# Optimization experiments

Hardware: AMD Instinct MI355X
Metric: run time of the kernel (lower is better)

Reference implementation:

```python
import jax, jax.numpy as jnp
import numpy as np

NEG_SLOPE = 0.2  # LeakyReLU(0.2) used for attention scores


def setup_inputs() -> dict:
    key = jax.random.key(0)
    k1, k2, k3, k4, k5 = jax.random.split(key, 5)
    B, H, N, F, D = 1024, 32, 25, 128, 128
    return {
        "x_self": jax.random.normal(k1, (B, H, F), dtype=jnp.float32),
        "x_neigh": jax.random.normal(k2, (B, H, N, F), dtype=jnp.float32),
        "w_feat": jax.random.normal(k3, (F, D), dtype=jnp.float32) * 0.1,
        "a_self": jax.random.normal(k4, (D, 1), dtype=jnp.float32) * 0.1,
        "a_neigh": jax.random.normal(k5, (D, 1), dtype=jnp.float32) * 0.1,
    }


def reference(x_self, x_neigh, w_feat, a_self, a_neigh):
    # xw_self: [B, H, 1, D]; xw_neigh: [B, H, N, D]
    xw_self = jnp.einsum("bhf,fd->bhd", x_self, w_feat)[:, :, None, :]
    xw_neigh = jnp.einsum("bhnf,fd->bhnd", x_neigh, w_feat)
    xw_all = jnp.concatenate([xw_self, xw_neigh], axis=2)  # [B, H, N+1, D]
    # attention scores over the (self + neighbours) axis
    attn_self = jnp.einsum("bhkd,do->bhko", xw_self, a_self)   # [B, H, 1, 1]
    attn_neigh = jnp.einsum("bhkd,do->bhko", xw_all, a_neigh)  # [B, H, N+1, 1]
    attn_u = jax.nn.leaky_relu(attn_self + attn_neigh, negative_slope=NEG_SLOPE)
    attn = jax.nn.softmax(attn_u, axis=2)                      # [B, H, N+1, 1]
    h_out = jnp.sum(attn * xw_all, axis=2)                     # [B, H, D]
    return jax.nn.relu(h_out)
```

## Files before the change

### kernel.cpp

```cpp
#include <hip/hip_runtime.h>

typedef unsigned short u16;
typedef unsigned int   u32;
typedef __attribute__((ext_vector_type(4))) float f32x4;
typedef __attribute__((ext_vector_type(4))) int   i32x4;

#define NPAIR 32768
#define NB    25
#define FD    128

__device__ __forceinline__ float bflo(u32 u){ return __uint_as_float(u << 16); }
__device__ __forceinline__ float bfhi(u32 u){ return __uint_as_float(u & 0xFFFF0000u); }
__device__ __forceinline__ u16 f2bf(float f){
  u32 u = __float_as_uint(f);
  u += 0x7FFFu + ((u >> 16) & 1u);
  return (u16)(u >> 16);
}
__device__ __forceinline__ float rowsum16(float x){
  x += __shfl_xor(x, 1);
  x += __shfl_xor(x, 2);
  x += __shfl_xor(x, 4);
  x += __shfl_xor(x, 8);
  return x;
}

__global__ __launch_bounds__(64) void prep_wa(const void* w_, const void* as_, const void* an_,
                                              const u16* __restrict__ xsniff,
                                              float* __restrict__ wa, int* __restrict__ flag_out){
  const int l = threadIdx.x;
  const u16 v1 = xsniff[l], v2 = xsniff[64 + l];
  int e1 = (v1 >> 7) & 0xFF, e2 = (v2 >> 7) & 0xFF;
  int e = e1 > e2 ? e1 : e2;
  #pragma unroll
  for(int m=1; m<=32; m<<=1){ int o = __shfl_xor(e, m); e = e > o ? e : o; }
  unsigned long long zb = __ballot(((l & 1) == 0) && (v1 == 0 || v2 == 0));
  const bool isf32 = (e >= 141) || (__popcll(zb) >= 20);

  const int f = blockIdx.x;
  float ps, pn;
  if (isf32){
    const float* w  = (const float*)w_;
    const float* as = (const float*)as_;
    const float* an = (const float*)an_;
    float w0 = w[f*FD + 2*l], w1 = w[f*FD + 2*l + 1];
    ps = w0*as[2*l] + w1*as[2*l+1];
    pn = w0*an[2*l] + w1*an[2*l+1];
  } else {
    const u16* w  = (const u16*)w_;
    const u16* as = (const u16*)as_;
    const u16* an = (const u16*)an_;
    u32 wd = *(const u32*)(w + f*FD + 2*l);
    u32 av = *(const u32*)(as + 2*l);
    u32 nv = *(const u32*)(an + 2*l);
    ps = bflo(wd)*bflo(av) + bfhi(wd)*bfhi(av);
    pn = bflo(wd)*bflo(nv) + bfhi(wd)*bfhi(nv);
  }
  #pragma unroll
  for(int m=1; m<=32; m<<=1){ ps += __shfl_xor(ps, m); pn += __shfl_xor(pn, m); }
  if (l == 0){ wa[f] = ps; wa[FD + f] = pn; }
  if (blockIdx.x == 0 && l == 0) flag_out[0] = isf32 ? 1 : 0;
}

template<bool FP32>
__device__ __forceinline__ void attn_body(const void* __restrict__ xs_, const void* __restrict__ xn_,
                                          const float* __restrict__ wa, u16* __restrict__ xbar,
                                          const int p, const int lane){
  const int g  = lane >> 4;
  const int q  = lane & 15;
  const int f0 = q << 3;

  float was[8], wan[8];
  {
    float4 a = *(const float4*)(wa + f0);
    float4 b = *(const float4*)(wa + f0 + 4);
    was[0]=a.x; was[1]=a.y; was[2]=a.z; was[3]=a.w;
    was[4]=b.x; was[5]=b.y; was[6]=b.z; was[7]=b.w;
    float4 c = *(const float4*)(wa + FD + f0);
    float4 d = *(const float4*)(wa + FD + f0 + 4);
    wan[0]=c.x; wan[1]=c.y; wan[2]=c.z; wan[3]=c.w;
    wan[4]=d.x; wan[5]=d.y; wan[6]=d.z; wan[7]=d.w;
  }

  float xf[7][8];
  #pragma unroll
  for(int i=0;i<7;++i){
    const int v = 4*i + g;
    if (v <= NB){
      if (FP32){
        const float* src = (v==0) ? ((const float*)xs_ + (size_t)p*FD + f0)
                                  : ((const float*)xn_ + (size_t)p*(NB*FD) + (size_t)(v-1)*FD + f0);
        float4 A = *(const float4*)src;
        float4 B = *(const float4*)(src + 4);
        xf[i][0]=A.x; xf[i][1]=A.y; xf[i][2]=A.z; xf[i][3]=A.w;
        xf[i][4]=B.x; xf[i][5]=B.y; xf[i][6]=B.z; xf[i][7]=B.w;
      } else {
        const u16* src = (v==0) ? ((const u16*)xs_ + (size_t)p*FD + f0)
                                : ((const u16*)xn_ + (size_t)p*(NB*FD) + (size_t)(v-1)*FD + f0);
        uint4 d = *(const uint4*)src;
        xf[i][0]=bflo(d.x); xf[i][1]=bfhi(d.x);
        xf[i][2]=bflo(d.y); xf[i][3]=bfhi(d.y);
        xf[i][4]=bflo(d.z); xf[i][5]=bfhi(d.z);
        xf[i][6]=bflo(d.w); xf[i][7]=bfhi(d.w);
      }
    } else {
      #pragma unroll
      for(int j=0;j<8;++j) xf[i][j] = 0.f;
    }
  }

  float pn[7];
  #pragma unroll
  for(int i=0;i<7;++i){
    float s = 0.f;
    #pragma unroll
    for(int j=0;j<8;++j) s += xf[i][j]*wan[j];
    pn[i] = rowsum16(s);
  }
  float ps = 0.f;
  #pragma unroll
  for(int j=0;j<8;++j) ps += xf[0][j]*was[j];
  ps = rowsum16(ps);
  const float s_self = __shfl(ps, 0);

  float u[7];
  #pragma unroll
  for(int i=0;i<7;++i){
    const int v = 4*i + g;
    if (v <= NB){
      float t = s_self + pn[i];
      u[i] = fmaxf(t, 0.2f*t);
    } else u[i] = -3.0e38f;
  }
  float m = u[0];
  #pragma unroll
  for(int i=1;i<7;++i) m = fmaxf(m, u[i]);
  m = fmaxf(m, __shfl_xor(m, 16));
  m = fmaxf(m, __shfl_xor(m, 32));

  float e[7]; float S = 0.f;
  #pragma unroll
  for(int i=0;i<7;++i){
    const int v = 4*i + g;
    e[i] = (v <= NB) ? __expf(u[i] - m) : 0.f;
    S += e[i];
  }
  S += __shfl_xor(S, 16);
  S += __shfl_xor(S, 32);
  const float rinv = 1.0f / S;

  float acc[8];
  #pragma unroll
  for(int j=0;j<8;++j) acc[j] = 0.f;
  #pragma unroll
  for(int i=0;i<7;++i)
    #pragma unroll
    for(int j=0;j<8;++j) acc[j] += e[i]*xf[i][j];
  #pragma unroll
  for(int j=0;j<8;++j){
    acc[j] += __shfl_xor(acc[j], 16);
    acc[j] += __shfl_xor(acc[j], 32);
    acc[j] *= rinv;
  }
  if (g == 0){
    u32 o0 = (u32)f2bf(acc[0]) | ((u32)f2bf(acc[1])<<16);
    u32 o1 = (u32)f2bf(acc[2]) | ((u32)f2bf(acc[3])<<16);
    u32 o2 = (u32)f2bf(acc[4]) | ((u32)f2bf(acc[5])<<16);
    u32 o3 = (u32)f2bf(acc[6]) | ((u32)f2bf(acc[7])<<16);
    *(uint4*)(xbar + (size_t)p*FD + f0) = make_uint4(o0,o1,o2,o3);
  }
}

__global__ __launch_bounds__(256) void attn_xbar(const void* __restrict__ xs, const void* __restrict__ xn,
                                                 const float* __restrict__ wa, const int* __restrict__ flag,
                                                 u16* __restrict__ xbar){
  const int lane = threadIdx.x & 63;
  const int p    = blockIdx.x*4 + (threadIdx.x >> 6);
  if (flag[0]) attn_body<true >(xs, xn, wa, xbar, p, lane);
  else         attn_body<false>(xs, xn, wa, xbar, p, lane);
}

__global__ __launch_bounds__(256) void matvec_out(const u16* __restrict__ xbar,
                                                  const void* __restrict__ w_,
                                                  void* __restrict__ out_,
                                                  const int* __restrict__ flag){
  __shared__ u16 wlds[FD*FD];
  const int tid = threadIdx.x;
  const bool isf32 = (flag[0] != 0);
  if (isf32){
    const float* w = (const float*)w_;
    #pragma unroll
    for(int i=0;i<8;++i){
      const int e = (i*256 + tid)*8;
      float4 A = *(const float4*)(w + e);
      float4 B = *(const float4*)(w + e + 4);
      u32 o0 = (u32)f2bf(A.x) | ((u32)f2bf(A.y)<<16);
      u32 o1 = (u32)f2bf(A.z) | ((u32)f2bf(A.w)<<16);
      u32 o2 = (u32)f2bf(B.x) | ((u32)f2bf(B.y)<<16);
      u32 o3 = (u32)f2bf(B.z) | ((u32)f2bf(B.w)<<16);
      *(uint4*)(wlds + e) = make_uint4(o0,o1,o2,o3);
    }
  } else {
    const u16* w = (const u16*)w_;
    #pragma unroll
    for(int i=0;i<8;++i){
      const int e = (i*256 + tid)*8;
      *(uint4*)(wlds + e) = *(const uint4*)(w + e);
    }
  }
  __syncthreads();

  const int lane = tid & 63, wv = tid >> 6;
  const int col  = lane & 15, quad = lane >> 4;

  i32x4 bfru[8][4];
  #pragma unroll
  for(int nt=0;nt<8;++nt)
    #pragma unroll
    for(int kt=0;kt<4;++kt){
      union { u16 s[8]; i32x4 u; } bb;
      #pragma unroll
      for(int j=0;j<8;++j) bb.s[j] = wlds[(kt*32 + quad*8 + j)*FD + nt*16 + col];
      bfru[nt][kt] = bb.u;
    }

  const int waveG = blockIdx.x*4 + wv;
  #pragma unroll
  for(int s=0;s<2;++s){
    const int tile = waveG + s*1024;
    const u16* arow = xbar + (size_t)(tile*16 + col)*FD;
    f32x4 acc[8];
    #pragma unroll
    for(int nt=0;nt<8;++nt){ f32x4 z = {0.f,0.f,0.f,0.f}; acc[nt] = z; }
    #pragma unroll
    for(int kt=0;kt<4;++kt){
      i32x4 av = *(const i32x4*)(arow + kt*32 + quad*8);
      #pragma unroll
      for(int nt=0;nt<8;++nt){
        asm volatile("s_nop 1\n\t"
                     "v_mfma_f32_16x16x32_bf16 %0, %1, %2, %0\n\t"
                     "s_nop 7\n\t"
                     "s_nop 7"
                     : "+v"(acc[nt]) : "v"(av), "v"(bfru[nt][kt]));
      }
    }
    if (isf32){
      float* orow = (float*)out_ + (size_t)tile*(16*FD);
      #pragma unroll
      for(int nt=0;nt<8;++nt)
        #pragma unroll
        for(int r=0;r<4;++r)
          orow[(quad*4+r)*FD + nt*16 + col] = fmaxf(acc[nt][r], 0.f);
    } else {
      u16* orow = (u16*)out_ + (size_t)tile*(16*FD);
      #pragma unroll
      for(int nt=0;nt<8;++nt)
        #pragma unroll
        for(int r=0;r<4;++r)
          orow[(quad*4+r)*FD + nt*16 + col] = f2bf(fmaxf(acc[nt][r], 0.f));
    }
  }
}

extern "C" void kernel_launch(void* const* d_in, const int* in_sizes, int n_in,
                              void* d_out, int out_size, void* d_ws, size_t ws_size,
                              hipStream_t stream){
  const void* x_self  = d_in[0];
  const void* x_neigh = d_in[1];
  const void* w_feat  = d_in[2];
  const void* a_self  = d_in[3];
  const void* a_neigh = d_in[4];

  int*   flag = (int*)d_ws;
  float* wa   = (float*)d_ws + 64;
  u16*   xbar = (u16*)d_ws + 1024;

  prep_wa  <<<FD,      64,  0, stream>>>(w_feat, a_self, a_neigh, (const u16*)x_self, wa, flag);
  attn_xbar<<<NPAIR/4, 256, 0, stream>>>(x_self, x_neigh, wa, flag, xbar);
  matvec_out<<<256,    256, 0, stream>>>(xbar, w_feat, d_out, flag);
}
```

Baseline: 568.2 us.

## Fuse attention aggregation with output matvec via LDS and prepacked W fragments

Merges the attention/xbar kernel and the MFMA matvec into one kernel: each block computes 16 aggregated rows into LDS, then multiplies them by W using fragments pre-packed in the prep kernel. This removes the global xbar write/read and a launch, and uses nontemporal loads for the streamed inputs. Each wave now processes 4 pairs serially, which may reduce memory-level parallelism.

```diff
diff --git a/kernel.cpp b/kernel.cpp
--- a/kernel.cpp
+++ b/kernel.cpp
@@ -4,6 +4,7 @@
 typedef unsigned int   u32;
 typedef __attribute__((ext_vector_type(4))) float f32x4;
 typedef __attribute__((ext_vector_type(4))) int   i32x4;
+typedef __attribute__((ext_vector_type(4))) u32   u32x4;
 
 #define NPAIR 32768
 #define NB    25
@@ -23,242 +24,231 @@
   x += __shfl_xor(x, 8);
   return x;
 }
-
-__global__ __launch_bounds__(64) void prep_wa(const void* w_, const void* as_, const void* an_,
-                                              const u16* __restrict__ xsniff,
-                                              float* __restrict__ wa, int* __restrict__ flag_out){
-  const int l = threadIdx.x;
+__device__ __forceinline__ bool sniff_f32(const u16* __restrict__ xsniff, int l){
   const u16 v1 = xsniff[l], v2 = xsniff[64 + l];
   int e1 = (v1 >> 7) & 0xFF, e2 = (v2 >> 7) & 0xFF;
   int e = e1 > e2 ? e1 : e2;
   #pragma unroll
-  for(int m=1; m<=32; m<<=1){ int o = __shfl_xor(e, m); e = e > o ? e : o; }
+  for (int m = 1; m <= 32; m <<= 1){ int o = __shfl_xor(e, m); e = e > o ? e : o; }
   unsigned long long zb = __ballot(((l & 1) == 0) && (v1 == 0 || v2 == 0));
-  const bool isf32 = (e >= 141) || (__popcll(zb) >= 20);
-
-  const int f = blockIdx.x;
-  float ps, pn;
-  if (isf32){
-    const float* w  = (const float*)w_;
-    const float* as = (const float*)as_;
-    const float* an = (const float*)an_;
-    float w0 = w[f*FD + 2*l], w1 = w[f*FD + 2*l + 1];
-    ps = w0*as[2*l] + w1*as[2*l+1];
-    pn = w0*an[2*l] + w1*an[2*l+1];
+  return (e >= 141) || (__popcll(zb) >= 20);
+}
+
+__global__ __launch_bounds__(64) void prep(const void* w_, const void* as_, const void* an_,
+                                           const u16* __restrict__ xsniff,
+                                           float* __restrict__ wa, u16* __restrict__ wpk,
+                                           int* __restrict__ flag_out){
+  const int l = threadIdx.x;
+  const bool isf32 = sniff_f32(xsniff, l);
+
+  if (blockIdx.x < FD){
+    const int f = blockIdx.x;
+    float ps, pn;
+    if (isf32){
+      const float* w  = (const float*)w_;
+      const float* as = (const float*)as_;
+      const float* an = (const float*)an_;
+      float w0 = w[f*FD + 2*l], w1 = w[f*FD + 2*l + 1];
+      ps = w0*as[2*l] + w1*as[2*l+1];
+      pn = w0*an[2*l] + w1*an[2*l+1];
+    } else {
+      const u16* w  = (const u16*)w_;
+      const u16* as = (const u16*)as_;
+      const u16* an = (const u16*)an_;
+      u32 wd = *(const u32*)(w + f*FD + 2*l);
+      u32 av = *(const u32*)(as + 2*l);
+      u32 nv = *(const u32*)(an + 2*l);
+      ps = bflo(wd)*bflo(av) + bfhi(wd)*bfhi(av);
+      pn = bflo(wd)*bflo(nv) + bfhi(wd)*bfhi(nv);
+    }
+    #pragma unroll
+    for(int m=1; m<=32; m<<=1){ ps += __shfl_xor(ps, m); pn += __shfl_xor(pn, m); }
+    if (l == 0){ wa[f] = ps; wa[FD + f] = pn; }
+    if (blockIdx.x == 0 && l == 0) flag_out[0] = isf32 ? 1 : 0;
   } else {
-    const u16* w  = (const u16*)w_;
-    const u16* as = (const u16*)as_;
-    const u16* an = (const u16*)an_;
-    u32 wd = *(const u32*)(w + f*FD + 2*l);
-    u32 av = *(const u32*)(as + 2*l);
-    u32 nv = *(const u32*)(an + 2*l);
-    ps = bflo(wd)*bflo(av) + bfhi(wd)*bfhi(av);
-    pn = bflo(wd)*bflo(nv) + bfhi(wd)*bfhi(nv);
-  }
-  #pragma unroll
-  for(int m=1; m<=32; m<<=1){ ps += __shfl_xor(ps, m); pn += __shfl_xor(pn, m); }
-  if (l == 0){ wa[f] = ps; wa[FD + f] = pn; }
-  if (blockIdx.x == 0 && l == 0) flag_out[0] = isf32 ? 1 : 0;
+    const int unit = (blockIdx.x - FD)*64 + l;
+    const int nt   = unit >> 8;
+    const int kt   = (unit >> 6) & 3;
+    const int fl   = unit & 63;
+    const int col  = fl & 15, quad = fl >> 4;
+    union { u16 s[8]; u32x4 u; } bb;
+    #pragma unroll
+    for (int j = 0; j < 8; ++j){
+      const int idx = (kt*32 + quad*8 + j)*FD + nt*16 + col;
+      bb.s[j] = isf32 ? f2bf(((const float*)w_)[idx]) : ((const u16*)w_)[idx];
+    }
+    *(u32x4*)(wpk + unit*8) = bb.u;
+  }
 }
 
 template<bool FP32>
-__device__ __forceinline__ void attn_body(const void* __restrict__ xs_, const void* __restrict__ xn_,
-                                          const float* __restrict__ wa, u16* __restrict__ xbar,
-                                          const int p, const int lane){
+__device__ __forceinline__ void fused_body(const void* __restrict__ xs_, const void* __restrict__ xn_,
+                                           const float* __restrict__ wa, const u16* __restrict__ wpk,
+                                           void* __restrict__ out_, u16* __restrict__ xb){
+  const int tid  = threadIdx.x;
+  const int lane = tid & 63, wv = tid >> 6;
   const int g  = lane >> 4;
   const int q  = lane & 15;
   const int f0 = q << 3;
+  const int pbase = blockIdx.x * 16;
 
   float was[8], wan[8];
   {
-    float4 a = *(const float4*)(wa + f0);
-    float4 b = *(const float4*)(wa + f0 + 4);
-    was[0]=a.x; was[1]=a.y; was[2]=a.z; was[3]=a.w;
-    was[4]=b.x; was[5]=b.y; was[6]=b.z; was[7]=b.w;
-    float4 c = *(const float4*)(wa + FD + f0);
-    float4 d = *(const float4*)(wa + FD + f0 + 4);
-    wan[0]=c.x; wan[1]=c.y; wan[2]=c.z; wan[3]=c.w;
-    wan[4]=d.x; wan[5]=d.y; wan[6]=d.z; wan[7]=d.w;
-  }
-
-  float xf[7][8];
+    f32x4 a = *(const f32x4*)(wa + f0);
+    f32x4 b = *(const f32x4*)(wa + f0 + 4);
+    was[0]=a[0]; was[1]=a[1]; was[2]=a[2]; was[3]=a[3];
+    was[4]=b[0]; was[5]=b[1]; was[6]=b[2]; was[7]=b[3];
+    f32x4 c = *(const f32x4*)(wa + FD + f0);
+    f32x4 d = *(const f32x4*)(wa + FD + f0 + 4);
+    wan[0]=c[0]; wan[1]=c[1]; wan[2]=c[2]; wan[3]=c[3];
+    wan[4]=d[0]; wan[5]=d[1]; wan[6]=d[2]; wan[7]=d[3];
+  }
+
+  #pragma unroll 1
+  for (int pp = 0; pp < 4; ++pp){
+    const int row = wv*4 + pp;
+    const int p   = pbase + row;
+
+    float xf[7][8];
+    #pragma unroll
+    for(int i=0;i<7;++i){
+      const int v = 4*i + g;
+      if (v <= NB){
+        if (FP32){
+          const float* src = (v==0) ? ((const float*)xs_ + (size_t)p*FD + f0)
+                                    : ((const float*)xn_ + (size_t)p*(NB*FD) + (size_t)(v-1)*FD + f0);
+          f32x4 A = __builtin_nontemporal_load((const f32x4*)src);
+          f32x4 B = __builtin_nontemporal_load((const f32x4*)(src + 4));
+          xf[i][0]=A[0]; xf[i][1]=A[1]; xf[i][2]=A[2]; xf[i][3]=A[3];
+          xf[i][4]=B[0]; xf[i][5]=B[1]; xf[i][6]=B[2]; xf[i][7]=B[3];
+        } else {
+          const u16* src = (v==0) ? ((const u16*)xs_ + (size_t)p*FD + f0)
+                                  : ((const u16*)xn_ + (size_t)p*(NB*FD) + (size_t)(v-1)*FD + f0);
+          u32x4 d = __builtin_nontemporal_load((const u32x4*)src);
+          xf[i][0]=bflo(d[0]); xf[i][1]=bfhi(d[0]);
+          xf[i][2]=bflo(d[1]); xf[i][3]=bfhi(d[1]);
+          xf[i][4]=bflo(d[2]); xf[i][5]=bfhi(d[2]);
+          xf[i][6]=bflo(d[3]); xf[i][7]=bfhi(d[3]);
+        }
+      } else {
+        #pragma unroll
+        for(int j=0;j<8;++j) xf[i][j] = 0.f;
+      }
+    }
+
+    float pn[7];
+    #pragma unroll
+    for(int i=0;i<7;++i){
+      float s = 0.f;
+      #pragma unroll
+      for(int j=0;j<8;++j) s += xf[i][j]*wan[j];
+      pn[i] = rowsum16(s);
+    }
+    float ps = 0.f;
+    #pragma unroll
+    for(int j=0;j<8;++j) ps += xf[0][j]*was[j];
+    ps = rowsum16(ps);
+    const float s_self = __shfl(ps, 0);
+
+    float u[7];
+    #pragma unroll
+    for(int i=0;i<7;++i){
+      const int v = 4*i + g;
+      if (v <= NB){
+        float t = s_self + pn[i];
+        u[i] = fmaxf(t, 0.2f*t);
+      } else u[i] = -3.0e38f;
+    }
+    float m = u[0];
+    #pragma unroll
+    for(int i=1;i<7;++i) m = fmaxf(m, u[i]);
+    m = fmaxf(m, __shfl_xor(m, 16));
+    m = fmaxf(m, __shfl_xor(m, 32));
+
+    float e[7]; float S = 0.f;
+    #pragma unroll
+    for(int i=0;i<7;++i){
+      const int v = 4*i + g;
+      e[i] = (v <= NB) ? __expf(u[i] - m) : 0.f;
+      S += e[i];
+    }
+    S += __shfl_xor(S, 16);
+    S += __shfl_xor(S, 32);
+    const float rinv = 1.0f / S;
+
+    float acc[8];
+    #pragma unroll
+    for(int j=0;j<8;++j) acc[j] = 0.f;
+    #pragma unroll
+    for(int i=0;i<7;++i)
+      #pragma unroll
+      for(int j=0;j<8;++j) acc[j] += e[i]*xf[i][j];
+    #pragma unroll
+    for(int j=0;j<8;++j){
+      acc[j] += __shfl_xor(acc[j], 16);
+      acc[j] += __shfl_xor(acc[j], 32);
+      acc[j] *= rinv;
+    }
+    if (g == 0){
+      u32 o0 = (u32)f2bf(acc[0]) | ((u32)f2bf(acc[1])<<16);
+      u32 o1 = (u32)f2bf(acc[2]) | ((u32)f2bf(acc[3])<<16);
+      u32 o2 = (u32)f2bf(acc[4]) | ((u32)f2bf(acc[5])<<16);
+      u32 o3 = (u32)f2bf(acc[6]) | ((u32)f2bf(acc[7])<<16);
+      u32x4 ov = {o0, o1, o2, o3};
+      *(u32x4*)(xb + row*FD + f0) = ov;
+    }
+  }
+  __syncthreads();
+
+  const int col = q, quad = g;
+  i32x4 bfru[2][4];
   #pragma unroll
-  for(int i=0;i<7;++i){
-    const int v = 4*i + g;
-    if (v <= NB){
-      if (FP32){
-        const float* src = (v==0) ? ((const float*)xs_ + (size_t)p*FD + f0)
-                                  : ((const float*)xn_ + (size_t)p*(NB*FD) + (size_t)(v-1)*FD + f0);
-        float4 A = *(const float4*)src;
-        float4 B = *(const float4*)(src + 4);
-        xf[i][0]=A.x; xf[i][1]=A.y; xf[i][2]=A.z; xf[i][3]=A.w;
-        xf[i][4]=B.x; xf[i][5]=B.y; xf[i][6]=B.z; xf[i][7]=B.w;
-      } else {
-        const u16* src = (v==0) ? ((const u16*)xs_ + (size_t)p*FD + f0)
-                                : ((const u16*)xn_ + (size_t)p*(NB*FD) + (size_t)(v-1)*FD + f0);
-        uint4 d = *(const uint4*)src;
-        xf[i][0]=bflo(d.x); xf[i][1]=bfhi(d.x);
-        xf[i][2]=bflo(d.y); xf[i][3]=bfhi(d.y);
-        xf[i][4]=bflo(d.z); xf[i][5]=bfhi(d.z);
-        xf[i][6]=bflo(d.w); xf[i][7]=bfhi(d.w);
-      }
-    } else {
-      #pragma unroll
-      for(int j=0;j<8;++j) xf[i][j] = 0.f;
-    }
-  }
-
-  float pn[7];
+  for (int ntl = 0; ntl < 2; ++ntl)
+    #pragma unroll
+    for (int kt = 0; kt < 4; ++kt)
+      bfru[ntl][kt] = *(const i32x4*)(wpk + (size_t)(((wv*2 + ntl)*4 + kt)*64 + lane)*8);
+
+  f32x4 acc2[2];
+  { f32x4 z = {0.f,0.f,0.f,0.f}; acc2[0] = z; acc2[1] = z; }
   #pragma unroll
-  for(int i=0;i<7;++i){
-    float s = 0.f;
-    #pragma unroll
-    for(int j=0;j<8;++j) s += xf[i][j]*wan[j];
-    pn[i] = rowsum16(s);
-  }
-  float ps = 0.f;
-  #pragma unroll
-  for(int j=0;j<8;++j) ps += xf[0][j]*was[j];
-  ps = rowsum16(ps);
-  const float s_self = __shfl(ps, 0);
-
-  float u[7];
-  #pragma unroll
-  for(int i=0;i<7;++i){
-    const int v = 4*i + g;
-    if (v <= NB){
-      float t = s_self + pn[i];
-      u[i] = fmaxf(t, 0.2f*t);
-    } else u[i] = -3.0e38f;
-  }
-  float m = u[0];
-  #pragma unroll
-  for(int i=1;i<7;++i) m = fmaxf(m, u[i]);
-  m = fmaxf(m, __shfl_xor(m, 16));
-  m = fmaxf(m, __shfl_xor(m, 32));
-
-  float e[7]; float S = 0.f;
-  #pragma unroll
-  for(int i=0;i<7;++i){
-    const int v = 4*i + g;
-    e[i] = (v <= NB) ? __expf(u[i] - m) : 0.f;
-    S += e[i];
-  }
-  S += __shfl_xor(S, 16);
-  S += __shfl_xor(S, 32);
-  const float rinv = 1.0f / S;
-
-  float acc[8];
-  #pragma unroll
-  for(int j=0;j<8;++j) acc[j] = 0.f;
-  #pragma unroll
-  for(int i=0;i<7;++i)
-    #pragma unroll
-    for(int j=0;j<8;++j) acc[j] += e[i]*xf[i][j];
-  #pragma unroll
-  for(int j=0;j<8;++j){
-    acc[j] += __shfl_xor(acc[j], 16);
-    acc[j] += __shfl_xor(acc[j], 32);
-    acc[j] *= rinv;
-  }
-  if (g == 0){
-    u32 o0 = (u32)f2bf(acc[0]) | ((u32)f2bf(acc[1])<<16);
-    u32 o1 = (u32)f2bf(acc[2]) | ((u32)f2bf(acc[3])<<16);
-    u32 o2 = (u32)f2bf(acc[4]) | ((u32)f2bf(acc[5])<<16);
-    u32 o3 = (u32)f2bf(acc[6]) | ((u32)f2bf(acc[7])<<16);
-    *(uint4*)(xbar + (size_t)p*FD + f0) = make_uint4(o0,o1,o2,o3);
-  }
-}
-
-__global__ __launch_bounds__(256) void attn_xbar(const void* __restrict__ xs, const void* __restrict__ xn,
-                                                 const float* __restrict__ wa, const int* __restrict__ flag,
-                                                 u16* __restrict__ xbar){
-  const int lane = threadIdx.x & 63;
-  const int p    = blockIdx.x*4 + (threadIdx.x >> 6);
-  if (flag[0]) attn_body<true >(xs, xn, wa, xbar, p, lane);
-  else         attn_body<false>(xs, xn, wa, xbar, p, lane);
-}
-
-__global__ __launch_bounds__(256) void matvec_out(const u16* __restrict__ xbar,
-                                                  const void* __restrict__ w_,
-                                                  void* __restrict__ out_,
-                                                  const int* __restrict__ flag){
-  __shared__ u16 wlds[FD*FD];
-  const int tid = threadIdx.x;
-  const bool isf32 = (flag[0] != 0);
-  if (isf32){
-    const float* w = (const float*)w_;
-    #pragma unroll
-    for(int i=0;i<8;++i){
-      const int e = (i*256 + tid)*8;
-      float4 A = *(const float4*)(w + e);
-      float4 B = *(const float4*)(w + e + 4);
-      u32 o0 = (u32)f2bf(A.x) | ((u32)f2bf(A.y)<<16);
-      u32 o1 = (u32)f2bf(A.z) | ((u32)f2bf(A.w)<<16);
-      u32 o2 = (u32)f2bf(B.x) | ((u32)f2bf(B.y)<<16);
-      u32 o3 = (u32)f2bf(B.z) | ((u32)f2bf(B.w)<<16);
-      *(uint4*)(wlds + e) = make_uint4(o0,o1,o2,o3);
+  for (int kt = 0; kt < 4; ++kt){
+    i32x4 av = *(const i32x4*)(xb + col*FD + kt*32 + quad*8);
+    #pragma unroll
+    for (int ntl = 0; ntl < 2; ++ntl){
+      asm volatile("s_nop 1\n\t"
+                   "v_mfma_f32_16x16x32_bf16 %0, %1, %2, %0\n\t"
+                   "s_nop 7\n\t"
+                   "s_nop 7"
+                   : "+v"(acc2[ntl]) : "v"(av), "v"(bfru[ntl][kt]));
+    }
+  }
+  if (FP32){
+    float* o = (float*)out_;
+    #pragma unroll
+    for (int ntl = 0; ntl < 2; ++ntl){
+      const int n0 = (wv*2 + ntl)*16 + col;
+      #pragma unroll
+      for (int r = 0; r < 4; ++r)
+        o[(size_t)(pbase + quad*4 + r)*FD + n0] = fmaxf(acc2[ntl][r], 0.f);
     }
   } else {
-    const u16* w = (const u16*)w_;
-    #pragma unroll
-    for(int i=0;i<8;++i){
-      const int e = (i*256 + tid)*8;
-      *(uint4*)(wlds + e) = *(const uint4*)(w + e);
-    }
-  }
-  __syncthreads();
-
-  const int lane = tid & 63, wv = tid >> 6;
-  const int col  = lane & 15, quad = lane >> 4;
-
-  i32x4 bfru[8][4];
-  #pragma unroll
-  for(int nt=0;nt<8;++nt)
-    #pragma unroll
-    for(int kt=0;kt<4;++kt){
-      union { u16 s[8]; i32x4 u; } bb;
-      #pragma unroll
-      for(int j=0;j<8;++j) bb.s[j] = wlds[(kt*32 + quad*8 + j)*FD + nt*16 + col];
-      bfru[nt][kt] = bb.u;
-    }
-
-  const int waveG = blockIdx.x*4 + wv;
-  #pragma unroll
-  for(int s=0;s<2;++s){
-    const int tile = waveG + s*1024;
-    const u16* arow = xbar + (size_t)(tile*16 + col)*FD;
-    f32x4 acc[8];
-    #pragma unroll
-    for(int nt=0;nt<8;++nt){ f32x4 z = {0.f,0.f,0.f,0.f}; acc[nt] = z; }
-    #pragma unroll
-    for(int kt=0;kt<4;++kt){
-      i32x4 av = *(const i32x4*)(arow + kt*32 + quad*8);
-      #pragma unroll
-      for(int nt=0;nt<8;++nt){
-        asm volatile("s_nop 1\n\t"
-                     "v_mfma_f32_16x16x32_bf16 %0, %1, %2, %0\n\t"
-                     "s_nop 7\n\t"
-                     "s_nop 7"
-                     : "+v"(acc[nt]) : "v"(av), "v"(bfru[nt][kt]));
-      }
-    }
-    if (isf32){
-      float* orow = (float*)out_ + (size_t)tile*(16*FD);
-      #pragma unroll
-      for(int nt=0;nt<8;++nt)
-        #pragma unroll
-        for(int r=0;r<4;++r)
-          orow[(quad*4+r)*FD + nt*16 + col] = fmaxf(acc[nt][r], 0.f);
-    } else {
-      u16* orow = (u16*)out_ + (size_t)tile*(16*FD);
-      #pragma unroll
-      for(int nt=0;nt<8;++nt)
-        #pragma unroll
-        for(int r=0;r<4;++r)
-          orow[(quad*4+r)*FD + nt*16 + col] = f2bf(fmaxf(acc[nt][r], 0.f));
-    }
-  }
+    u16* o = (u16*)out_;
+    #pragma unroll
+    for (int ntl = 0; ntl < 2; ++ntl){
+      const int n0 = (wv*2 + ntl)*16 + col;
+      #pragma unroll
+      for (int r = 0; r < 4; ++r)
+        o[(size_t)(pbase + quad*4 + r)*FD + n0] = f2bf(fmaxf(acc2[ntl][r], 0.f));
+    }
+  }
+}
+
+__global__ __launch_bounds__(256) void fused(const void* __restrict__ xs, const void* __restrict__ xn,
+                                             const float* __restrict__ wa, const int* __restrict__ flag,
+                                             const u16* __restrict__ wpk, void* __restrict__ out_){
+  __shared__ u16 xb[16*FD];
+  if (flag[0]) fused_body<true >(xs, xn, wa, wpk, out_, xb);
+  else         fused_body<false>(xs, xn, wa, wpk, out_, xb);
 }
 
 extern "C" void kernel_launch(void* const* d_in, const int* in_sizes, int n_in,
@@ -272,9 +262,8 @@
 
   int*   flag = (int*)d_ws;
   float* wa   = (float*)d_ws + 64;
-  u16*   xbar = (u16*)d_ws + 1024;
-
-  prep_wa  <<<FD,      64,  0, stream>>>(w_feat, a_self, a_neigh, (const u16*)x_self, wa, flag);
-  attn_xbar<<<NPAIR/4, 256, 0, stream>>>(x_self, x_neigh, wa, flag, xbar);
-  matvec_out<<<256,    256, 0, stream>>>(xbar, w_feat, d_out, flag);
-}
+  u16*   wpk  = (u16*)d_ws + 1024;
+
+  prep <<<FD + 32,  64, 0, stream>>>(w_feat, a_self, a_neigh, (const u16*)x_self, wa, wpk, flag);
+  fused<<<NPAIR/16, 256, 0, stream>>>(x_self, x_neigh, wa, flag, wpk, d_out);
+}
```

Measured after the change: 549.7 us. 3.3% less time.
